# Kernel optimization log

Hardware: AMD Instinct MI355X
Metric: run time of the kernel (lower is better)

## Reference

```python
import jax, jax.numpy as jnp
import numpy as np

N = 50000   # nodes
E = 600000  # edges (time_feat is per-edge: same mask indexes k and src_idx)
D = 128     # adapter_dim
C = 8       # num_clusters
SCALE = D ** -0.5


def setup_inputs() -> dict:
    key = jax.random.key(0)
    ks = jax.random.split(key, 12)
    s = 1.0 / np.sqrt(D)
    return {
        "node_feat": jax.random.normal(ks[0], (N, D), jnp.float32),
        "time_feat": jax.random.normal(ks[1], (E, D), jnp.float32),
        "context_feat": jax.random.normal(ks[2], (N, D), jnp.float32),
        "edge_index": jax.random.randint(ks[3], (2, E), 0, N),
        "Wq": jax.random.uniform(ks[4], (D, D), jnp.float32, -s, s),
        "bq": jnp.zeros((D,), jnp.float32),
        "Wk": jax.random.uniform(ks[5], (D, D), jnp.float32, -s, s),
        "bk": jnp.zeros((D,), jnp.float32),
        "Wv": jax.random.uniform(ks[6], (D, D), jnp.float32, -s, s),
        "bv": jnp.zeros((D,), jnp.float32),
        "cluster_emb": jax.random.normal(ks[7], (C, D), jnp.float32),
        "Wo": jax.random.uniform(ks[8], (D, D), jnp.float32, -s, s),
        "bo": jnp.zeros((D,), jnp.float32),
    }


def reference(node_feat, time_feat, context_feat, edge_index,
              Wq, bq, Wk, bk, Wv, bv, cluster_emb, Wo, bo):
    q = node_feat @ Wq + bq            # [N, D]
    k = time_feat @ Wk + bk            # [E, D]
    v = time_feat @ Wv + bv            # [E, D]

    # cluster routing: argmax(softmax(sim)) == argmax(sim)
    sim = (time_feat @ cluster_emb.T) * SCALE   # [E, C]
    assign = jnp.argmax(sim, axis=-1)           # [E] int

    src = edge_index[0]                          # [E]
    seg = assign * N + src                       # combined (cluster, dst-of-scatter) segment id
    nseg = C * N

    attn = jnp.sum(q[src] * k, axis=-1) * SCALE  # [E]

    # scatter_softmax per (cluster, src node)
    seg_max = jax.ops.segment_max(attn, seg, num_segments=nseg)
    ex = jnp.exp(attn - seg_max[seg])
    denom = jax.ops.segment_sum(ex, seg, num_segments=nseg)
    w = ex / denom[seg]                          # [E]

    # scatter_mean per (cluster, src node) -> [C, N, D]
    wv = v * w[:, None]
    sums = jax.ops.segment_sum(wv, seg, num_segments=nseg)                 # [C*N, D]
    counts = jax.ops.segment_sum(jnp.ones((E,), v.dtype), seg, num_segments=nseg)
    means = sums / jnp.maximum(counts, 1.0)[:, None]                       # empty -> 0
    per_cluster = means.reshape(C, N, D)

    # sum(outputs) / len(outputs): only non-empty clusters contribute an entry
    edges_per_cluster = jax.ops.segment_sum(jnp.ones((E,), jnp.float32), assign, num_segments=C)
    num_nonempty = jnp.sum((edges_per_cluster > 0).astype(jnp.float32))
    combined = per_cluster.sum(axis=0) / num_nonempty                      # [N, D]

    return jax.nn.relu(combined @ Wo + bo)
```

## Files before the change

kernel.cpp:

```cpp
#include <hip/hip_runtime.h>
#include <math.h>


#define NN 50000
#define NE 600000
#define DD 128
#define NC 8
#define WIN 64
#define NWIN 9376
#define NBF  9377
#define EC 84
#define NLOC 32
#define SCALEF 0.08838834764831845f

#define OFF_NODECNT  0
#define OFF_FILL     50000
#define OFF_MASK     100000
#define ZERO_ELEMS   100256
#define OFF_NODEOFF  100352
#define OFF_PARTIAL  150352
#define OFF_BF       150608
#define OFF_BQK      160000
#define OFF_BVO      160128
#define OFF_WQBK     160256
#define OFF_C0       160384
#define OFF_WQK      160400
#define OFF_WVO      176784
#define OFF_QB       193168
#define OFF_SORTED   243168
#define OFF_SRCS     843168
#define OFF_SW       1443168
#define OFF_P        1493168

__global__ __launch_bounds__(256) void k_pre_count(
    const float* __restrict__ Wq, const float* __restrict__ bq,
    const float* __restrict__ Wk, const float* __restrict__ bk,
    const float* __restrict__ Wv, const float* __restrict__ bv,
    const float* __restrict__ Wo, const int* __restrict__ ei,
    int* __restrict__ node_cnt,
    float* __restrict__ Wqk, float* __restrict__ bqk,
    float* __restrict__ Wvo, float* __restrict__ bvo,
    float* __restrict__ wqbk, float* __restrict__ c0) {
  int bid = blockIdx.x, t = threadIdx.x;
  if (bid >= 129) {
    long e = (long)(bid - 129) * 256 + t;
    if (e < NE) atomicAdd(&node_cnt[ei[e]], 1);
    return;
  }
  __shared__ float rq[DD], rv[DD];
  int b = bid;
  if (b < DD) {
    if (t < DD) { rq[t] = Wq[b * DD + t]; rv[t] = Wv[b * DD + t]; }
    __syncthreads();
    if (t < DD) {
      float aq = 0.f, av = 0.f;
      for (int j = 0; j < DD; j++) {
        aq += rq[j] * Wk[t * DD + j];
        av += rv[j] * Wo[j * DD + t];
      }
      Wqk[b * DD + t] = aq;
      Wvo[b * DD + t] = av;
    }
  } else {
    if (t < DD) {
      float a1 = 0.f, a2 = 0.f, a3 = 0.f;
      for (int j = 0; j < DD; j++) {
        a1 += bq[j] * Wk[t * DD + j];
        a2 += bv[j] * Wo[j * DD + t];
        a3 += Wq[t * DD + j] * bk[j];
      }
      bqk[t] = a1; bvo[t] = a2; wqbk[t] = a3;
      if (t == 0) {
        float s = 0.f;
        for (int j = 0; j < DD; j++) s += bq[j] * bk[j];
        *c0 = s;
      }
    }
  }
}

__global__ __launch_bounds__(256) void k_p(
    const float* __restrict__ nf, const float* __restrict__ Wqk,
    const float* __restrict__ bqk, const float* __restrict__ wqbk,
    const float* __restrict__ c0p,
    float* __restrict__ p, float* __restrict__ qb) {
  __shared__ float a_lds[64 * DD];
  __shared__ float wb_lds[DD];
  int t = threadIdx.x;
  long row0 = (long)blockIdx.x * 64;
  for (int it = 0; it < 8; it++) {
    int idx = (it * 256 + t) * 4;
    long r = row0 + idx / DD;
    float4 v = {0.f, 0.f, 0.f, 0.f};
    if (r < NN) v = *(const float4*)(nf + r * DD + (idx % DD));
    *(float4*)(a_lds + idx) = v;
  }
  if (t < DD) wb_lds[t] = wqbk[t];
  __syncthreads();
  int cg = t % 32, rg = t / 32;
  int col0 = cg * 4, r0 = rg * 8;
  float acc[8][4]; float qacc[8];
  for (int r = 0; r < 8; r++) { qacc[r] = 0.f; for (int c = 0; c < 4; c++) acc[r][c] = 0.f; }
  for (int k = 0; k < DD; k++) {
    float4 b4 = *(const float4*)(Wqk + k * DD + col0);
    float wbk = wb_lds[k];
    for (int r = 0; r < 8; r++) {
      float a = a_lds[(r0 + r) * DD + k];
      acc[r][0] += a * b4.x; acc[r][1] += a * b4.y;
      acc[r][2] += a * b4.z; acc[r][3] += a * b4.w;
      qacc[r] += a * wbk;
    }
  }
  float4 bq4 = *(const float4*)(bqk + col0);
  float c0v = *c0p;
  for (int r = 0; r < 8; r++) {
    long row = row0 + r0 + r;
    if (row < NN) {
      float4 o;
      o.x = acc[r][0] + bq4.x; o.y = acc[r][1] + bq4.y;
      o.z = acc[r][2] + bq4.z; o.w = acc[r][3] + bq4.w;
      *(float4*)(p + row * DD + col0) = o;
      if (cg == 0) qb[row] = qacc[r] + c0v;
    }
  }
}

__global__ __launch_bounds__(256) void k_scan1(const int* __restrict__ node_cnt,
                                               int* __restrict__ partial) {
  int i = blockIdx.x * 256 + threadIdx.x;
  int v = (i < NN) ? node_cnt[i] : 0;
  for (int o = 1; o < 64; o <<= 1) v += __shfl_xor(v, o);
  __shared__ int wsum[4];
  if ((threadIdx.x & 63) == 0) wsum[threadIdx.x >> 6] = v;
  __syncthreads();
  if (threadIdx.x == 0) partial[blockIdx.x] = wsum[0] + wsum[1] + wsum[2] + wsum[3];
}

__global__ __launch_bounds__(256) void k_scan2(int* __restrict__ partial) {
  __shared__ int s[256];
  int t = threadIdx.x;
  int v = (t < 196) ? partial[t] : 0;
  s[t] = v;
  __syncthreads();
  for (int o = 1; o < 256; o <<= 1) {
    int add = (t >= o) ? s[t - o] : 0;
    __syncthreads();
    s[t] += add;
    __syncthreads();
  }
  if (t < 196) partial[t] = s[t] - v;
}

__global__ __launch_bounds__(256) void k_scan3(const int* __restrict__ node_cnt,
                                               const int* __restrict__ partial,
                                               int* __restrict__ node_off) {
  __shared__ int s[256];
  int t = threadIdx.x;
  int i = blockIdx.x * 256 + t;
  int v = (i < NN) ? node_cnt[i] : 0;
  s[t] = v;
  __syncthreads();
  for (int o = 1; o < 256; o <<= 1) {
    int add = (t >= o) ? s[t - o] : 0;
    __syncthreads();
    s[t] += add;
    __syncthreads();
  }
  if (i < NN) node_off[i] = partial[blockIdx.x] + s[t] - v;
}

#define EDGE_BLKS 2344
#define BS_BLKS   37
__global__ __launch_bounds__(256) void k_scatter(const int* __restrict__ ei,
                                                 const int* __restrict__ node_off,
                                                 int* __restrict__ fill,
                                                 int* __restrict__ sorted,
                                                 int* __restrict__ srcs,
                                                 int* __restrict__ blockFirst) {
  int bid = blockIdx.x, t = threadIdx.x;
  if (bid >= EDGE_BLKS) {
    int w = (bid - EDGE_BLKS) * 256 + t;
    if (w < NBF) {
      int v = w * WIN, lo = 0, hi = NN;
      while (lo < hi) { int mid = (lo + hi) >> 1; if (node_off[mid] < v) lo = mid + 1; else hi = mid; }
      blockFirst[w] = lo;
    }
    return;
  }
  long e = (long)bid * 256 + t;
  if (e < NE) {
    int s = ei[e];
    int pos = node_off[s] + atomicAdd(&fill[s], 1);
    sorted[pos] = (int)e;
    srcs[pos] = s;
  }
}

__device__ __forceinline__ void phase_a(
    const float* __restrict__ tf, const float* __restrict__ p,
    const float* __restrict__ qb,
    const float* ce_lds, float* t_lds, float* exf_sh, int* cli_sh,
    float* D_sh, int* C_sh,
    int el, int j, int eid, int src, int lnode, bool doStage, bool doDC) {
  const float* trow = tf + (long)eid * DD;
  float4 tv[8];
  #pragma unroll
  for (int i = 0; i < 8; i++) tv[i] = *(const float4*)(trow + (j * 8 + i) * 4);
  if (doStage) {
    int e7 = el & 7;
    #pragma unroll
    for (int i = 0; i < 8; i++)
      *(float4*)(t_lds + el * DD + (((j * 8 + i) ^ e7) << 2)) = tv[i];
  }
  const float* prow = p + (long)src * DD;
  float a = 0.f;
  #pragma unroll
  for (int i = 0; i < 8; i++) {
    float4 pv = *(const float4*)(prow + (j * 8 + i) * 4);
    a += tv[i].x * pv.x + tv[i].y * pv.y + tv[i].z * pv.z + tv[i].w * pv.w;
  }
  float sims[NC];
  #pragma unroll
  for (int c = 0; c < NC; c++) {
    const float* cr = ce_lds + c * DD;
    float s = 0.f;
    #pragma unroll
    for (int i = 0; i < 8; i++) {
      float4 cv = *(const float4*)(cr + (j * 8 + i) * 4);
      s += tv[i].x * cv.x + tv[i].y * cv.y + tv[i].z * cv.z + tv[i].w * cv.w;
    }
    sims[c] = s;
  }
  #pragma unroll
  for (int c = 0; c < NC; c++) {
    sims[c] += __shfl_xor(sims[c], 1);
    sims[c] += __shfl_xor(sims[c], 2);
  }
  a += __shfl_xor(a, 1);
  a += __shfl_xor(a, 2);
  if (j == 0) {
    float best = sims[0]; int bc = 0;
    #pragma unroll
    for (int c = 1; c < NC; c++) if (sims[c] > best) { best = sims[c]; bc = c; }
    float ex = expf((a + qb[src]) * SCALEF);
    exf_sh[el] = ex; cli_sh[el] = bc;
    if (doDC) {
      atomicAdd(&D_sh[lnode * NC + bc], ex);
      atomicAdd(&C_sh[lnode * NC + bc], 1);
    }
  }
}

__global__ __launch_bounds__(256) void k_fused3(
    const float* __restrict__ tf, const int* __restrict__ sorted,
    const int* __restrict__ srcs, const int* __restrict__ node_off,
    const int* __restrict__ node_cnt, const int* __restrict__ blockFirst,
    const float* __restrict__ ce, const float* __restrict__ p,
    const float* __restrict__ qb, int* __restrict__ maskArr,
    float* __restrict__ agg, float* __restrict__ sw) {
  __shared__ float t_lds[EC * DD];
  __shared__ float ce_lds[NC * DD];
  __shared__ float exf_sh[EC];
  __shared__ float scl_sh[EC];
  __shared__ int   cli_sh[EC];
  __shared__ int   eidx_sh[EC];
  __shared__ int   srcs_sh[EC];
  __shared__ int   offL_sh[NLOC];
  __shared__ int   cntL_sh[NLOC];
  __shared__ float D_sh[NLOC * NC];
  __shared__ int   C_sh[NLOC * NC];
  __shared__ int   ctrl[4];

  int t = threadIdx.x, b = blockIdx.x;
  int fn = blockFirst[b], ln = blockFirst[b + 1] - 1;
  if (fn >= NN || ln < fn) return;

  *(float4*)(ce_lds + t * 4) = *(const float4*)(ce + t * 4);

  int el4 = t >> 2, j4 = t & 3;
  int team = t >> 6, d2 = (t & 63) * 2;
  int msk = 0;

  int s0 = fn;
  while (s0 <= ln) {
    if (t < 64) {
      int offv = 0, cntv = 0; bool fit = false;
      if (t < NLOC && s0 + t <= ln) { offv = node_off[s0 + t]; cntv = node_cnt[s0 + t]; }
      int off0 = __shfl(offv, 0);
      if (t < NLOC && s0 + t <= ln) fit = (offv - off0 + cntv) <= EC;
      unsigned long long bm = __ballot(fit);
      int pref = (int)__popcll(bm);
      if (t < pref) { offL_sh[t] = offv - off0; cntL_sh[t] = cntv; }
      if (t == 0) { ctrl[0] = pref; ctrl[2] = off0; ctrl[3] = cntv; }
      if (pref > 0 && t == pref - 1) ctrl[1] = offv - off0 + cntv;
    }
    for (int i = t; i < NLOC * NC; i += 256) { D_sh[i] = 0.f; C_sh[i] = 0; }
    __syncthreads();
    int nN = ctrl[0], eb = ctrl[2];

    if (nN == 0) {
      int cnt = ctrl[3];
      for (int c0 = 0; c0 < cnt; c0 += 64) {
        int m = cnt - c0; if (m > 64) m = 64;
        if (t < m) eidx_sh[t] = sorted[eb + c0 + t];
        __syncthreads();
        if (el4 < m)
          phase_a(tf, p, qb, ce_lds, t_lds, exf_sh, cli_sh, D_sh, C_sh,
                  el4, j4, eidx_sh[el4], s0, 0, false, true);
        __syncthreads();
      }
      float r0a = 0.f, r1a = 0.f;
      for (int c0 = 0; c0 < cnt; c0 += EC) {
        int m = cnt - c0; if (m > EC) m = EC;
        if (t < m) eidx_sh[t] = sorted[eb + c0 + t];
        __syncthreads();
        for (int r0 = 0; r0 < m; r0 += 64) {
          int el = r0 + el4;
          if (el < m)
            phase_a(tf, p, qb, ce_lds, t_lds, exf_sh, cli_sh, D_sh, C_sh,
                    el, j4, eidx_sh[el], s0, 0, true, false);
        }
        __syncthreads();
        if (t < m) {
          int c = cli_sh[t];
          scl_sh[t] = exf_sh[t] * __builtin_amdgcn_rcpf(D_sh[c] * (float)C_sh[c]);
        }
        __syncthreads();
        for (int e = team; e < m; e += 4) {
          float s = scl_sh[e];
          const float* tp = t_lds + e * DD + ((((d2 >> 2) ^ (e & 7)) << 2) | (d2 & 3));
          r0a += s * tp[0]; r1a += s * tp[1];
        }
        __syncthreads();
      }
      *(float2*)(t_lds + team * DD + d2) = make_float2(r0a, r1a);
      __syncthreads();
      if (team == 0) {
        float s0v = 0.f, s1v = 0.f;
        #pragma unroll
        for (int tm = 0; tm < 4; tm++) {
          s0v += t_lds[tm * DD + d2]; s1v += t_lds[tm * DD + d2 + 1];
        }
        *(float2*)(agg + (long)s0 * DD + d2) = make_float2(s0v, s1v);
      }
      if (t == 0) {
        float ssw = 0.f; int mk = 0;
        #pragma unroll
        for (int c = 0; c < NC; c++) {
          int cc = C_sh[c];
          if (cc > 0) { mk |= 1 << c; ssw += __builtin_amdgcn_rcpf((float)cc); }
        }
        sw[s0] = ssw; msk |= mk;
      }
      __syncthreads();
      s0 += 1;
      continue;
    }

    int span = ctrl[1];
    if (t < span) { eidx_sh[t] = sorted[eb + t]; srcs_sh[t] = srcs[eb + t]; }
    __syncthreads();

    for (int r0 = 0; r0 < span; r0 += 64) {
      int el = r0 + el4;
      if (el < span) {
        int src = srcs_sh[el];
        phase_a(tf, p, qb, ce_lds, t_lds, exf_sh, cli_sh, D_sh, C_sh,
                el, j4, eidx_sh[el], src, src - s0, true, true);
      }
    }
    __syncthreads();

    if (t < span) {
      int l = (srcs_sh[t] - s0) * NC + cli_sh[t];
      scl_sh[t] = exf_sh[t] * __builtin_amdgcn_rcpf(D_sh[l] * (float)C_sh[l]);
    }
    __syncthreads();

    for (int k = team; k < nN; k += 4) {
      float r0a = 0.f, r1a = 0.f;
      int e1 = offL_sh[k] + cntL_sh[k];
      for (int e = offL_sh[k]; e < e1; e++) {
        float s = scl_sh[e];
        const float* tp = t_lds + e * DD + ((((d2 >> 2) ^ (e & 7)) << 2) | (d2 & 3));
        r0a += s * tp[0]; r1a += s * tp[1];
      }
      long n = s0 + k;
      *(float2*)(agg + n * DD + d2) = make_float2(r0a, r1a);
      if ((t & 63) == 0) {
        float ssw = 0.f; int mk = 0;
        #pragma unroll
        for (int c = 0; c < NC; c++) {
          int cc = C_sh[k * NC + c];
          if (cc > 0) { mk |= 1 << c; ssw += __builtin_amdgcn_rcpf((float)cc); }
        }
        sw[n] = ssw; msk |= mk;
      }
    }
    __syncthreads();
    s0 += nN;
  }
  if (msk) atomicOr(&maskArr[b & 255], msk);
}

__global__ __launch_bounds__(256) void k_out(
    const float* __restrict__ agg, const float* __restrict__ Wvo,
    const float* __restrict__ bvo, const float* __restrict__ sw,
    const float* __restrict__ bo, const int* __restrict__ maskArr,
    float* __restrict__ out) {
  __shared__ float a_lds[64 * DD];
  __shared__ float sw_lds[64];
  __shared__ int morw[4];
  int t = threadIdx.x;
  int mv = maskArr[t];
  for (int o = 1; o < 64; o <<= 1) mv |= __shfl_xor(mv, o);
  if ((t & 63) == 0) morw[t >> 6] = mv;
  long row0 = (long)blockIdx.x * 64;
  for (int it = 0; it < 8; it++) {
    int idx = (it * 256 + t) * 4;
    long r = row0 + idx / DD;
    float4 v = {0.f, 0.f, 0.f, 0.f};
    if (r < NN) v = *(const float4*)(agg + r * DD + (idx % DD));
    *(float4*)(a_lds + idx) = v;
  }
  if (t < 64) {
    long r = row0 + t;
    sw_lds[t] = (r < NN) ? sw[r] : 0.f;
  }
  __syncthreads();
  int full = morw[0] | morw[1] | morw[2] | morw[3];
  int nne = __popc(full); if (nne == 0) nne = 1;
  float inv = 1.0f / (float)nne;
  int cg = t % 32, rg = t / 32;
  int col0 = cg * 4, r0 = rg * 8;
  float acc[8][4];
  for (int r = 0; r < 8; r++) for (int c = 0; c < 4; c++) acc[r][c] = 0.f;
  for (int k = 0; k < DD; k++) {
    float4 b4 = *(const float4*)(Wvo + k * DD + col0);
    for (int r = 0; r < 8; r++) {
      float a = a_lds[(r0 + r) * DD + k];
      acc[r][0] += a * b4.x; acc[r][1] += a * b4.y;
      acc[r][2] += a * b4.z; acc[r][3] += a * b4.w;
    }
  }
  float4 bv4 = *(const float4*)(bvo + col0);
  float4 bo4 = *(const float4*)(bo + col0);
  for (int r = 0; r < 8; r++) {
    long row = row0 + r0 + r;
    if (row < NN) {
      float s = sw_lds[r0 + r];
      float4 o;
      o.x = fmaxf((acc[r][0] + s * bv4.x) * inv + bo4.x, 0.f);
      o.y = fmaxf((acc[r][1] + s * bv4.y) * inv + bo4.y, 0.f);
      o.z = fmaxf((acc[r][2] + s * bv4.z) * inv + bo4.z, 0.f);
      o.w = fmaxf((acc[r][3] + s * bv4.w) * inv + bo4.w, 0.f);
      *(float4*)(out + row * DD + col0) = o;
    }
  }
}

extern "C" void kernel_launch(void* const* d_in, const int* in_sizes, int n_in,
                              void* d_out, int out_size, void* d_ws, size_t ws_size,
                              hipStream_t stream) {
  const float* nf = (const float*)d_in[0];
  const float* tf = (const float*)d_in[1];
  const int*   ei = (const int*)d_in[3];
  const float* Wq = (const float*)d_in[4];
  const float* bq = (const float*)d_in[5];
  const float* Wk = (const float*)d_in[6];
  const float* bk = (const float*)d_in[7];
  const float* Wv = (const float*)d_in[8];
  const float* bv = (const float*)d_in[9];
  const float* ce = (const float*)d_in[10];
  const float* Wo = (const float*)d_in[11];
  const float* bo = (const float*)d_in[12];
  float* out = (float*)d_out;

  float* ws  = (float*)d_ws;
  int*   node_cnt = (int*)(ws + OFF_NODECNT);
  int*   fill     = (int*)(ws + OFF_FILL);
  int*   maskArr  = (int*)(ws + OFF_MASK);
  int*   node_off = (int*)(ws + OFF_NODEOFF);
  int*   partial  = (int*)(ws + OFF_PARTIAL);
  int*   blockFirst = (int*)(ws + OFF_BF);
  float* bqk      = ws + OFF_BQK;
  float* bvo      = ws + OFF_BVO;
  float* wqbk     = ws + OFF_WQBK;
  float* c0       = ws + OFF_C0;
  float* Wqk      = ws + OFF_WQK;
  float* Wvo      = ws + OFF_WVO;
  float* qb       = ws + OFF_QB;
  int*   sorted   = (int*)(ws + OFF_SORTED);
  int*   srcs     = (int*)(ws + OFF_SRCS);
  float* sw       = ws + OFF_SW;
  float* p        = ws + OFF_P;
  float* agg      = ws + OFF_P;

  hipMemsetAsync(d_ws, 0, (size_t)ZERO_ELEMS * 4, stream);

  k_pre_count<<<129 + EDGE_BLKS, 256, 0, stream>>>(
      Wq, bq, Wk, bk, Wv, bv, Wo, ei, node_cnt, Wqk, bqk, Wvo, bvo, wqbk, c0);
  k_p<<<(NN + 63) / 64, 256, 0, stream>>>(nf, Wqk, bqk, wqbk, c0, p, qb);
  k_scan1<<<196, 256, 0, stream>>>(node_cnt, partial);
  k_scan2<<<1, 256, 0, stream>>>(partial);
  k_scan3<<<196, 256, 0, stream>>>(node_cnt, partial, node_off);
  k_scatter<<<EDGE_BLKS + BS_BLKS, 256, 0, stream>>>(ei, node_off, fill, sorted,
                                                     srcs, blockFirst);
  k_fused3<<<NWIN, 256, 0, stream>>>(tf, sorted, srcs, node_off, node_cnt,
                                     blockFirst, ce, p, qb, maskArr, agg, sw);
  k_out<<<(NN + 63) / 64, 256, 0, stream>>>(agg, Wvo, bvo, sw, bo, maskArr, out);
}
```

Measured before the change: 688.5 us.

## Use eight lanes per edge, shrink edge tile, stage qb in LDS

The fused edge kernel now gives each edge to 8 lanes instead of 4, with an interleaved float4 pattern so the row loads coalesce better. The edge-tile capacity drops from 84 to 60 to cut LDS use and raise occupancy. Edge ids and sources are read straight from global memory instead of being staged in LDS, and per-node qb values are cached in shared memory. The aggregation uses 8 teams that each accumulate a float4 column slice. Smaller tiles mean more windows take the slow single-node fallback path, and the extra shuffle step adds cost per edge.

```diff
diff --git a/kernel.cpp b/kernel.cpp
--- a/kernel.cpp
+++ b/kernel.cpp
@@ -9,7 +9,7 @@
 #define WIN 64
 #define NWIN 9376
 #define NBF  9377
-#define EC 84
+#define EC 60
 #define NLOC 32
 #define SCALEF 0.08838834764831845f
 
@@ -198,25 +198,25 @@
 
 __device__ __forceinline__ void phase_a(
     const float* __restrict__ tf, const float* __restrict__ p,
-    const float* __restrict__ qb,
     const float* ce_lds, float* t_lds, float* exf_sh, int* cli_sh,
     float* D_sh, int* C_sh,
-    int el, int j, int eid, int src, int lnode, bool doStage, bool doDC) {
+    int slot, int j, int eid, int src, int lnode, float qbv,
+    bool doStage, bool doDC) {
   const float* trow = tf + (long)eid * DD;
-  float4 tv[8];
+  float4 tv[4];
   #pragma unroll
-  for (int i = 0; i < 8; i++) tv[i] = *(const float4*)(trow + (j * 8 + i) * 4);
+  for (int i = 0; i < 4; i++) tv[i] = *(const float4*)(trow + (i * 8 + j) * 4);
   if (doStage) {
-    int e7 = el & 7;
+    int e7 = slot & 7;
     #pragma unroll
-    for (int i = 0; i < 8; i++)
-      *(float4*)(t_lds + el * DD + (((j * 8 + i) ^ e7) << 2)) = tv[i];
+    for (int i = 0; i < 4; i++)
+      *(float4*)(t_lds + slot * DD + (((i * 8 + j) ^ e7) << 2)) = tv[i];
   }
   const float* prow = p + (long)src * DD;
   float a = 0.f;
   #pragma unroll
-  for (int i = 0; i < 8; i++) {
-    float4 pv = *(const float4*)(prow + (j * 8 + i) * 4);
+  for (int i = 0; i < 4; i++) {
+    float4 pv = *(const float4*)(prow + (i * 8 + j) * 4);
     a += tv[i].x * pv.x + tv[i].y * pv.y + tv[i].z * pv.z + tv[i].w * pv.w;
   }
   float sims[NC];
@@ -225,8 +225,8 @@
     const float* cr = ce_lds + c * DD;
     float s = 0.f;
     #pragma unroll
-    for (int i = 0; i < 8; i++) {
-      float4 cv = *(const float4*)(cr + (j * 8 + i) * 4);
+    for (int i = 0; i < 4; i++) {
+      float4 cv = *(const float4*)(cr + (i * 8 + j) * 4);
       s += tv[i].x * cv.x + tv[i].y * cv.y + tv[i].z * cv.z + tv[i].w * cv.w;
     }
     sims[c] = s;
@@ -235,15 +235,17 @@
   for (int c = 0; c < NC; c++) {
     sims[c] += __shfl_xor(sims[c], 1);
     sims[c] += __shfl_xor(sims[c], 2);
+    sims[c] += __shfl_xor(sims[c], 4);
   }
   a += __shfl_xor(a, 1);
   a += __shfl_xor(a, 2);
+  a += __shfl_xor(a, 4);
   if (j == 0) {
     float best = sims[0]; int bc = 0;
     #pragma unroll
     for (int c = 1; c < NC; c++) if (sims[c] > best) { best = sims[c]; bc = c; }
-    float ex = expf((a + qb[src]) * SCALEF);
-    exf_sh[el] = ex; cli_sh[el] = bc;
+    float ex = expf((a + qbv) * SCALEF);
+    exf_sh[slot] = ex; cli_sh[slot] = bc;
     if (doDC) {
       atomicAdd(&D_sh[lnode * NC + bc], ex);
       atomicAdd(&C_sh[lnode * NC + bc], 1);
@@ -251,7 +253,7 @@
   }
 }
 
-__global__ __launch_bounds__(256) void k_fused3(
+__global__ __launch_bounds__(256) void k_fused4(
     const float* __restrict__ tf, const int* __restrict__ sorted,
     const int* __restrict__ srcs, const int* __restrict__ node_off,
     const int* __restrict__ node_cnt, const int* __restrict__ blockFirst,
@@ -263,10 +265,9 @@
   __shared__ float exf_sh[EC];
   __shared__ float scl_sh[EC];
   __shared__ int   cli_sh[EC];
-  __shared__ int   eidx_sh[EC];
-  __shared__ int   srcs_sh[EC];
   __shared__ int   offL_sh[NLOC];
   __shared__ int   cntL_sh[NLOC];
+  __shared__ float qb_sh[NLOC];
   __shared__ float D_sh[NLOC * NC];
   __shared__ int   C_sh[NLOC * NC];
   __shared__ int   ctrl[4];
@@ -277,21 +278,24 @@
 
   *(float4*)(ce_lds + t * 4) = *(const float4*)(ce + t * 4);
 
-  int el4 = t >> 2, j4 = t & 3;
-  int team = t >> 6, d2 = (t & 63) * 2;
+  int el8 = t >> 3, j8 = t & 7;
+  int team = t >> 5, c4 = t & 31;
   int msk = 0;
 
   int s0 = fn;
   while (s0 <= ln) {
     if (t < 64) {
       int offv = 0, cntv = 0; bool fit = false;
-      if (t < NLOC && s0 + t <= ln) { offv = node_off[s0 + t]; cntv = node_cnt[s0 + t]; }
+      bool valid = (t < NLOC && s0 + t <= ln);
+      if (valid) { offv = node_off[s0 + t]; cntv = node_cnt[s0 + t]; }
       int off0 = __shfl(offv, 0);
-      if (t < NLOC && s0 + t <= ln) fit = (offv - off0 + cntv) <= EC;
+      if (valid) {
+        fit = (offv - off0 + cntv) <= EC;
+        offL_sh[t] = offv - off0; cntL_sh[t] = cntv; qb_sh[t] = qb[s0 + t];
+      }
       unsigned long long bm = __ballot(fit);
       int pref = (int)__popcll(bm);
-      if (t < pref) { offL_sh[t] = offv - off0; cntL_sh[t] = cntv; }
-      if (t == 0) { ctrl[0] = pref; ctrl[2] = off0; ctrl[3] = cntv; }
+      if (t == 0) { ctrl[0] = pref; ctrl[2] = off0; }
       if (pref > 0 && t == pref - 1) ctrl[1] = offv - off0 + cntv;
     }
     for (int i = t; i < NLOC * NC; i += 256) { D_sh[i] = 0.f; C_sh[i] = 0; }
@@ -299,26 +303,23 @@
     int nN = ctrl[0], eb = ctrl[2];
 
     if (nN == 0) {
-      int cnt = ctrl[3];
-      for (int c0 = 0; c0 < cnt; c0 += 64) {
-        int m = cnt - c0; if (m > 64) m = 64;
-        if (t < m) eidx_sh[t] = sorted[eb + c0 + t];
-        __syncthreads();
-        if (el4 < m)
-          phase_a(tf, p, qb, ce_lds, t_lds, exf_sh, cli_sh, D_sh, C_sh,
-                  el4, j4, eidx_sh[el4], s0, 0, false, true);
-        __syncthreads();
-      }
-      float r0a = 0.f, r1a = 0.f;
+      int cnt = cntL_sh[0];
+      float qbv0 = qb_sh[0];
+      for (int c0 = 0; c0 < cnt; c0 += 32) {
+        int el = c0 + el8;
+        if (el < cnt)
+          phase_a(tf, p, ce_lds, t_lds, exf_sh, cli_sh, D_sh, C_sh,
+                  el8, j8, sorted[eb + el], s0, 0, qbv0, false, true);
+      }
+      __syncthreads();
+      float4 r = {0.f, 0.f, 0.f, 0.f};
       for (int c0 = 0; c0 < cnt; c0 += EC) {
         int m = cnt - c0; if (m > EC) m = EC;
-        if (t < m) eidx_sh[t] = sorted[eb + c0 + t];
-        __syncthreads();
-        for (int r0 = 0; r0 < m; r0 += 64) {
-          int el = r0 + el4;
-          if (el < m)
-            phase_a(tf, p, qb, ce_lds, t_lds, exf_sh, cli_sh, D_sh, C_sh,
-                    el, j4, eidx_sh[el], s0, 0, true, false);
+        for (int r0 = 0; r0 < m; r0 += 32) {
+          int sl = r0 + el8;
+          if (sl < m)
+            phase_a(tf, p, ce_lds, t_lds, exf_sh, cli_sh, D_sh, C_sh,
+                    sl, j8, sorted[eb + c0 + sl], s0, 0, qbv0, true, false);
         }
         __syncthreads();
         if (t < m) {
@@ -326,22 +327,20 @@
           scl_sh[t] = exf_sh[t] * __builtin_amdgcn_rcpf(D_sh[c] * (float)C_sh[c]);
         }
         __syncthreads();
-        for (int e = team; e < m; e += 4) {
+        for (int e = team; e < m; e += 8) {
           float s = scl_sh[e];
-          const float* tp = t_lds + e * DD + ((((d2 >> 2) ^ (e & 7)) << 2) | (d2 & 3));
-          r0a += s * tp[0]; r1a += s * tp[1];
+          const float4 tv = *(const float4*)(t_lds + e * DD + ((c4 ^ (e & 7)) << 2));
+          r.x += s * tv.x; r.y += s * tv.y; r.z += s * tv.z; r.w += s * tv.w;
         }
         __syncthreads();
       }
-      *(float2*)(t_lds + team * DD + d2) = make_float2(r0a, r1a);
+      *(float4*)(t_lds + team * DD + c4 * 4) = r;
       __syncthreads();
-      if (team == 0) {
-        float s0v = 0.f, s1v = 0.f;
+      if (t < DD) {
+        float acc = 0.f;
         #pragma unroll
-        for (int tm = 0; tm < 4; tm++) {
-          s0v += t_lds[tm * DD + d2]; s1v += t_lds[tm * DD + d2 + 1];
-        }
-        *(float2*)(agg + (long)s0 * DD + d2) = make_float2(s0v, s1v);
+        for (int tm = 0; tm < 8; tm++) acc += t_lds[tm * DD + t];
+        agg[(long)s0 * DD + t] = acc;
       }
       if (t == 0) {
         float ssw = 0.f; int mk = 0;
@@ -358,36 +357,35 @@
     }
 
     int span = ctrl[1];
-    if (t < span) { eidx_sh[t] = sorted[eb + t]; srcs_sh[t] = srcs[eb + t]; }
-    __syncthreads();
-
-    for (int r0 = 0; r0 < span; r0 += 64) {
-      int el = r0 + el4;
+
+    for (int r0 = 0; r0 < span; r0 += 32) {
+      int el = r0 + el8;
       if (el < span) {
-        int src = srcs_sh[el];
-        phase_a(tf, p, qb, ce_lds, t_lds, exf_sh, cli_sh, D_sh, C_sh,
-                el, j4, eidx_sh[el], src, src - s0, true, true);
+        int src = srcs[eb + el];
+        phase_a(tf, p, ce_lds, t_lds, exf_sh, cli_sh, D_sh, C_sh,
+                el, j8, sorted[eb + el], src, src - s0, qb_sh[src - s0],
+                true, true);
       }
     }
     __syncthreads();
 
     if (t < span) {
-      int l = (srcs_sh[t] - s0) * NC + cli_sh[t];
+      int l = (srcs[eb + t] - s0) * NC + cli_sh[t];
       scl_sh[t] = exf_sh[t] * __builtin_amdgcn_rcpf(D_sh[l] * (float)C_sh[l]);
     }
     __syncthreads();
 
-    for (int k = team; k < nN; k += 4) {
-      float r0a = 0.f, r1a = 0.f;
+    for (int k = team; k < nN; k += 8) {
+      float4 r = {0.f, 0.f, 0.f, 0.f};
       int e1 = offL_sh[k] + cntL_sh[k];
       for (int e = offL_sh[k]; e < e1; e++) {
         float s = scl_sh[e];
-        const float* tp = t_lds + e * DD + ((((d2 >> 2) ^ (e & 7)) << 2) | (d2 & 3));
-        r0a += s * tp[0]; r1a += s * tp[1];
+        const float4 tv = *(const float4*)(t_lds + e * DD + ((c4 ^ (e & 7)) << 2));
+        r.x += s * tv.x; r.y += s * tv.y; r.z += s * tv.z; r.w += s * tv.w;
       }
       long n = s0 + k;
-      *(float2*)(agg + n * DD + d2) = make_float2(r0a, r1a);
-      if ((t & 63) == 0) {
+      *(float4*)(agg + n * DD + c4 * 4) = r;
+      if (c4 == 0) {
         float ssw = 0.f; int mk = 0;
         #pragma unroll
         for (int c = 0; c < NC; c++) {
@@ -400,7 +398,7 @@
     __syncthreads();
     s0 += nN;
   }
-  if (msk) atomicOr(&maskArr[b & 255], msk);
+  if ((t & 31) == 0 && msk) atomicOr(&maskArr[b & 255], msk);
 }
 
 __global__ __launch_bounds__(256) void k_out(
@@ -506,7 +504,7 @@
   k_scan3<<<196, 256, 0, stream>>>(node_cnt, partial, node_off);
   k_scatter<<<EDGE_BLKS + BS_BLKS, 256, 0, stream>>>(ei, node_off, fill, sorted,
                                                      srcs, blockFirst);
-  k_fused3<<<NWIN, 256, 0, stream>>>(tf, sorted, srcs, node_off, node_cnt,
+  k_fused4<<<NWIN, 256, 0, stream>>>(tf, sorted, srcs, node_off, node_cnt,
                                      blockFirst, ce, p, qb, maskArr, agg, sw);
   k_out<<<(NN + 63) / 64, 256, 0, stream>>>(agg, Wvo, bvo, sw, bo, maskArr, out);
 }
```

After: 688.7 us. Within noise of the previous version (+0.0%).
